# Kernel tuning notes

Hardware: AMD Instinct MI355X
Metric: run time of the kernel (lower is better)

Reference implementation:

```python
import jax, jax.numpy as jnp
import numpy as np

B, N, K = 64, 1024, 10   # graphs, nodes per graph, kNN neighbors
SLOPE = 0.01             # LeakyReLU default negative slope


def lrelu(v):
    return jnp.where(v >= 0, v, SLOPE * v)


def setup_inputs() -> dict:
    key = jax.random.key(0)
    ks = jax.random.split(key, 12)

    def w(k, shape):
        fan_in = shape[0]
        return jax.random.normal(k, shape, jnp.float32) * (1.0 / np.sqrt(fan_in))

    return {
        "x":   jax.random.normal(ks[0], (B * N, 1), jnp.float32),
        "pos": jax.random.normal(ks[1], (B * N, 3), jnp.float32),
        "tq":  jax.random.normal(ks[2], (B * N, 1), jnp.float32),
        # uniform, sorted graph assignment (B graphs of N nodes each)
        "batch": jnp.repeat(jnp.arange(B, dtype=jnp.int32), N),
        "W1":   w(ks[3], (10, 64)),  "b1":  jnp.zeros((64,), jnp.float32),
        "W2":   w(ks[4], (128, 64)), "b2":  jnp.zeros((64,), jnp.float32),
        "Wl1a": w(ks[5], (384, 512)), "bl1a": jnp.zeros((512,), jnp.float32),
        "Wl1b": w(ks[6], (512, 512)), "bl1b": jnp.zeros((512,), jnp.float32),
        "Wm1":  w(ks[7], (512, 256)), "bm1": jnp.zeros((256,), jnp.float32),
        "Wm2":  w(ks[8], (256, 3)),   "bm2": jnp.zeros((3,), jnp.float32),
    }


def _dynamic_edge_conv(h, W, b):
    # h: [B, N, F]. Dynamic kNN in feature space (per graph, self included,
    # matching PyG knn(x, x, k)), then sum_j LeakyReLU(Linear([x_i, x_j - x_i])).
    sq = jnp.sum(h * h, axis=-1)                                   # [B,N]
    dist = sq[:, :, None] + sq[:, None, :] - 2.0 * jnp.einsum("bif,bjf->bij", h, h)
    idx = jax.lax.top_k(-dist, K)[1]                               # [B,N,K] int32
    hj = jax.vmap(lambda hb, ib: hb[ib])(h, idx)                   # [B,N,K,F]
    hi = jnp.broadcast_to(h[:, :, None, :], hj.shape)
    e = jnp.concatenate([hi, hj - hi], axis=-1)                    # [B,N,K,2F]
    msg = lrelu(jnp.einsum("bnkf,fo->bnko", e, W) + b)             # [B,N,K,64]
    return jnp.sum(msg, axis=2)                                    # 'add' aggregation


def reference(x, pos, tq, batch, W1, b1, W2, b2,
              Wl1a, bl1a, Wl1b, bl1b, Wm1, bm1, Wm2, bm2):
    # batch is uniform & sorted: reshape to [B, N, .] realizes per-graph grouping.
    xx = jnp.concatenate([tq, x, pos], axis=1).reshape(B, N, 5)
    h1 = _dynamic_edge_conv(xx, W1, b1)
    h2 = _dynamic_edge_conv(h1, W2, b2)   # conv2 reused with shared weights
    h3 = _dynamic_edge_conv(h2, W2, b2)
    h4 = _dynamic_edge_conv(h3, W2, b2)
    h5 = _dynamic_edge_conv(h4, W2, b2)
    h6 = _dynamic_edge_conv(h5, W2, b2)
    hc = jnp.concatenate([h1, h2, h3, h4, h5, h6], axis=-1)        # [B,N,384]
    out0 = lrelu(hc @ Wl1a + bl1a) @ Wl1b + bl1b                   # [B,N,512]
    pooled = jnp.max(out0, axis=1)                                 # global_max_pool -> [B,512]
    return lrelu(pooled @ Wm1 + bm1) @ Wm2 + bm2                   # [B,3]
```

## Files before the change

### kernel.cpp

```cpp
#include <hip/hip_runtime.h>
#include <cstdint>
#include <cstddef>

constexpr int Bg = 64;
constexpr int Nn = 1024;
constexpr int Kk = 10;
constexpr int BN = Bg * Nn;
#define SLOPE 0.01f

typedef __attribute__((ext_vector_type(8))) short s16x8;
typedef __attribute__((ext_vector_type(4))) float f32x4;

__device__ __forceinline__ float lrelu(float v) { return v >= 0.f ? v : SLOPE * v; }

__device__ __forceinline__ unsigned encf(float f) {
  unsigned u = __float_as_uint(f);
  return (u & 0x80000000u) ? ~u : (u | 0x80000000u);
}
__device__ __forceinline__ float decf(unsigned e) {
  unsigned u = (e & 0x80000000u) ? (e & 0x7fffffffu) : ~e;
  return __uint_as_float(u);
}
__device__ __forceinline__ unsigned short f2bf(float f) {
  unsigned u = __float_as_uint(f);
  return (unsigned short)((u + 0x7FFFu + ((u >> 16) & 1u)) >> 16);
}
__device__ __forceinline__ float bf2f(unsigned short h) {
  return __uint_as_float(((unsigned)h) << 16);
}

__device__ __forceinline__ f32x4 mfma16(s16x8 a, s16x8 b, f32x4 c) {
  return __builtin_amdgcn_mfma_f32_16x16x32_bf16(a, b, c, 0, 0, 0);
}

__global__ __launch_bounds__(256) void pooled_init(unsigned* __restrict__ p) {
  p[blockIdx.x * 256 + threadIdx.x] = 0u;
}

__global__ __launch_bounds__(256) void build_xx(const float* __restrict__ x,
                                                const float* __restrict__ pos,
                                                const float* __restrict__ tq,
                                                float* __restrict__ xx,
                                                float* __restrict__ sqn, int rowoff) {
  int n = blockIdx.x * 256 + threadIdx.x;
  int g = rowoff + n;
  float v0 = tq[g], v1 = x[g];
  float v2 = pos[g * 3 + 0], v3 = pos[g * 3 + 1], v4 = pos[g * 3 + 2];
  xx[n * 5 + 0] = v0;
  xx[n * 5 + 1] = v1;
  xx[n * 5 + 2] = v2;
  xx[n * 5 + 3] = v3;
  xx[n * 5 + 4] = v4;
  float s0 = v0 * v0, s1 = v1 * v1, s2 = v2 * v2, s3 = v3 * v3, s4 = v4 * v4;
  sqn[n] = ((s0 + s4) + s2) + (s1 + s3);
}

template <int K>
__global__ __launch_bounds__(256) void wprep(const float* __restrict__ W,
                                             short* __restrict__ WH,
                                             short* __restrict__ WL) {
  int idx = blockIdx.x * 256 + threadIdx.x;
  int k = idx >> 9, n = idx & 511;
  float v = W[idx];
  unsigned short h = f2bf(v);
  unsigned short lo = f2bf(v - bf2f(h));
  WH[(size_t)n * K + k] = (short)h;
  WL[(size_t)n * K + k] = (short)lo;
}

template <int F>
__global__ __launch_bounds__(256) void uv_kernel(const float* __restrict__ h,
                                                 const float* __restrict__ W,
                                                 float* __restrict__ U,
                                                 float* __restrict__ V) {
  __shared__ float Ws[2 * F * 64];
  __shared__ float hs[16 * F];
  const int t = threadIdx.x;
  const int n0 = blockIdx.x * 16;
  for (int l = t; l < 2 * F * 64; l += 256) Ws[l] = W[l];
  for (int l = t; l < 16 * F; l += 256) hs[l] = h[(size_t)n0 * F + l];
  __syncthreads();
  for (int l = t; l < F * 64; l += 256) Ws[l] = Ws[l] - Ws[F * 64 + l];
  __syncthreads();
  const int o = t & 63;
  #pragma unroll
  for (int g4 = 0; g4 < 16; g4 += 4) {
    const int g = g4 + (t >> 6);
    float u = 0.f, v = 0.f;
    for (int f = 0; f < F; ++f) {
      float hv = hs[g * F + f];
      u += hv * Ws[f * 64 + o];
      v += hv * Ws[F * 64 + f * 64 + o];
    }
    U[(size_t)(n0 + g) * 64 + o] = u;
    V[(size_t)(n0 + g) * 64 + o] = v;
  }
}

#define LADDER_STATE                                                                     \
  float bd0 = INFINITY, bd1 = INFINITY, bd2 = INFINITY, bd3 = INFINITY, bd4 = INFINITY,  \
        bd5 = INFINITY, bd6 = INFINITY, bd7 = INFINITY, bd8 = INFINITY, bd9 = INFINITY;  \
  int bj0 = 0x7fffffff, bj1 = 0x7fffffff, bj2 = 0x7fffffff, bj3 = 0x7fffffff,            \
      bj4 = 0x7fffffff, bj5 = 0x7fffffff, bj6 = 0x7fffffff, bj7 = 0x7fffffff,            \
      bj8 = 0x7fffffff, bj9 = 0x7fffffff;

#define LADDER_INS                                                                        \
  auto ins = [&](float kd, int kj) {                                                      \
    bool m0 = kd < bd0; bool m1 = kd < bd1; bool m2 = kd < bd2; bool m3 = kd < bd3;       \
    bool m4 = kd < bd4; bool m5 = kd < bd5; bool m6 = kd < bd6; bool m7 = kd < bd7;       \
    bool m8 = kd < bd8; bool m9 = kd < bd9;                                               \
    bd9 = m8 ? bd8 : (m9 ? kd : bd9); bj9 = m8 ? bj8 : (m9 ? kj : bj9);                   \
    bd8 = m7 ? bd7 : (m8 ? kd : bd8); bj8 = m7 ? bj7 : (m8 ? kj : bj8);                   \
    bd7 = m6 ? bd6 : (m7 ? kd : bd7); bj7 = m6 ? bj6 : (m7 ? kj : bj7);                   \
    bd6 = m5 ? bd5 : (m6 ? kd : bd6); bj6 = m5 ? bj5 : (m6 ? kj : bj6);                   \
    bd5 = m4 ? bd4 : (m5 ? kd : bd5); bj5 = m4 ? bj4 : (m5 ? kj : bj5);                   \
    bd4 = m3 ? bd3 : (m4 ? kd : bd4); bj4 = m3 ? bj3 : (m4 ? kj : bj4);                   \
    bd3 = m2 ? bd2 : (m3 ? kd : bd3); bj3 = m2 ? bj2 : (m3 ? kj : bj3);                   \
    bd2 = m1 ? bd1 : (m2 ? kd : bd2); bj2 = m1 ? bj1 : (m2 ? kj : bj2);                   \
    bd1 = m0 ? bd0 : (m1 ? kd : bd1); bj1 = m0 ? bj0 : (m1 ? kj : bj1);                   \
    bd0 = m0 ? kd : bd0;              bj0 = m0 ? kj : bj0;                                \
  };

#define FMA16(av, bv)                                                        \
  do {                                                                       \
    acc[0][0] += av.x * bv.x; acc[0][1] += av.x * bv.y;                      \
    acc[0][2] += av.x * bv.z; acc[0][3] += av.x * bv.w;                      \
    acc[1][0] += av.y * bv.x; acc[1][1] += av.y * bv.y;                      \
    acc[1][2] += av.y * bv.z; acc[1][3] += av.y * bv.w;                      \
    acc[2][0] += av.z * bv.x; acc[2][1] += av.z * bv.y;                      \
    acc[2][2] += av.z * bv.z; acc[2][3] += av.z * bv.w;                      \
    acc[3][0] += av.w * bv.x; acc[3][1] += av.w * bv.y;                      \
    acc[3][2] += av.w * bv.z; acc[3][3] += av.w * bv.w;                      \
  } while (0)

template <int F>
__global__ __launch_bounds__(256) void knn_kernel(const float* __restrict__ h,
                                                  const float* __restrict__ sqn,
                                                  int* __restrict__ idxout) {
  constexpr int IPB = 64;
  constexpr int TJ = 64;
  constexpr int LDA = 68;
  constexpr int LDD = 65;
  constexpr int LDM = 41;
  constexpr int UNI = (IPB * LDM * 2 > TJ * LDA) ? IPB * LDM * 2 : TJ * LDA;
  __shared__ float As[F][LDA];
  __shared__ float uni[UNI];
  __shared__ float sqt[TJ];
  float* Bs = uni;
  float* D  = uni;
  float* md = uni;
  int*   mi = (int*)(uni + IPB * LDM);

  const int b = blockIdx.y;
  const int i0 = blockIdx.x * IPB;
  const int t = threadIdx.x;
  const int tx = t & 15, ty = t >> 4;
  const int gbase = b * Nn;
  const int r = t & 63;
  const int s = t >> 6;

  for (int l = t; l < IPB * F; l += 256) {
    int row = l / F, f = l % F;
    As[f][row] = h[(size_t)(gbase + i0 + row) * F + f];
  }

  LADDER_STATE
  LADDER_INS

  for (int jt = 0; jt < Nn; jt += TJ) {
    __syncthreads();
    for (int l = t; l < TJ * F; l += 256) {
      int row = l / F, f = l % F;
      Bs[f * LDA + row] = h[(size_t)(gbase + jt + row) * F + f];
    }
    if (t < TJ) sqt[t] = sqn[gbase + jt + t];
    __syncthreads();

    float acc[4][4] = {{0.f, 0.f, 0.f, 0.f}, {0.f, 0.f, 0.f, 0.f},
                       {0.f, 0.f, 0.f, 0.f}, {0.f, 0.f, 0.f, 0.f}};
    #pragma unroll
    for (int f = 0; f < F; ++f) {
      float4 av = *(const float4*)&As[f][ty * 4];
      float4 bv = *(const float4*)(Bs + f * LDA + tx * 4);
      FMA16(av, bv);
    }
    __syncthreads();

    float4 sj = *(const float4*)&sqt[tx * 4];
    #pragma unroll
    for (int ii = 0; ii < 4; ++ii) {
      float* dr = D + (ty * 4 + ii) * LDD + tx * 4;
      dr[0] = sj.x - 2.f * acc[ii][0];
      dr[1] = sj.y - 2.f * acc[ii][1];
      dr[2] = sj.z - 2.f * acc[ii][2];
      dr[3] = sj.w - 2.f * acc[ii][3];
    }
    __syncthreads();

    {
      const float* drow = D + r * LDD + s * 16;
      float dv[16];
      #pragma unroll
      for (int qq = 0; qq < 16; ++qq) dv[qq] = drow[qq];
      #pragma unroll
      for (int qq = 0; qq < 16; ++qq) ins(dv[qq], jt + s * 16 + qq);
    }
  }

  __syncthreads();
  {
    float* rd = md + r * LDM + s * 10;
    int*   ri = mi + r * LDM + s * 10;
    rd[0] = bd0; rd[1] = bd1; rd[2] = bd2; rd[3] = bd3; rd[4] = bd4;
    rd[5] = bd5; rd[6] = bd6; rd[7] = bd7; rd[8] = bd8; rd[9] = bd9;
    ri[0] = bj0; ri[1] = bj1; ri[2] = bj2; ri[3] = bj3; ri[4] = bj4;
    ri[5] = bj5; ri[6] = bj6; ri[7] = bj7; ri[8] = bj8; ri[9] = bj9;
  }
  __syncthreads();
  if (s == 0) {
    float* rd = md + r * LDM;
    int*   ri = mi + r * LDM;
    #pragma unroll 1
    for (int q = 0; q < Kk; ++q) {
      float best = INFINITY;
      int besti = 0x7fffffff, bslot = 0;
      #pragma unroll 1
      for (int e = 0; e < 40; ++e) {
        float d = rd[e];
        int ix = ri[e];
        bool g = (d < best) || (d == best && ix < besti);
        if (g) { best = d; besti = ix; bslot = e; }
      }
      rd[bslot] = INFINITY;
      idxout[(size_t)(gbase + i0 + r) * Kk + q] = besti;
    }
  }
}

__global__ __launch_bounds__(256) void knn64_mfma(const short* __restrict__ hH,
                                                  const short* __restrict__ hL,
                                                  const float* __restrict__ sqn,
                                                  int* __restrict__ idxout) {
  constexpr int LDB = 72;
  constexpr int LDD = 65;
  constexpr int LDM = 41;
  __shared__ float uni[64 * LDM * 2];
  __shared__ float sqt[64];
  short* BHs = (short*)uni;
  short* BLs = (short*)uni + 64 * LDB;
  float* D   = uni;
  float* md  = uni;
  int*   mi  = (int*)(uni + 64 * LDM);

  const int b = blockIdx.y;
  const int i0 = blockIdx.x * 64;
  const int t = threadIdx.x;
  const int w = t >> 6, l = t & 63;
  const int rl = l & 15, kb = l >> 4;
  const int gbase = b * Nn;

  s16x8 aH0, aH1, aL0, aL1;
  {
    const size_t ar = (size_t)(gbase + i0 + w * 16 + rl) * 64;
    aH0 = *(const s16x8*)&hH[ar + kb * 8];
    aH1 = *(const s16x8*)&hH[ar + 32 + kb * 8];
    aL0 = *(const s16x8*)&hL[ar + kb * 8];
    aL1 = *(const s16x8*)&hL[ar + 32 + kb * 8];
  }

  LADDER_STATE
  LADDER_INS

  uint4 pH0, pH1, pL0, pL1;
  {
    const size_t rb = (size_t)(gbase + l) * 64;
    pH0 = *(const uint4*)&hH[rb + w * 8];
    pH1 = *(const uint4*)&hH[rb + (w + 4) * 8];
    pL0 = *(const uint4*)&hL[rb + w * 8];
    pL1 = *(const uint4*)&hL[rb + (w + 4) * 8];
  }

  for (int jt = 0; jt < Nn; jt += 64) {
    __syncthreads();
    *(uint4*)&BHs[l * LDB + w * 8]       = pH0;
    *(uint4*)&BHs[l * LDB + (w + 4) * 8] = pH1;
    *(uint4*)&BLs[l * LDB + w * 8]       = pL0;
    *(uint4*)&BLs[l * LDB + (w + 4) * 8] = pL1;
    if (t < 64) sqt[t] = sqn[gbase + jt + t];
    if (jt + 64 < Nn) {
      const size_t rb = (size_t)(gbase + jt + 64 + l) * 64;
      pH0 = *(const uint4*)&hH[rb + w * 8];
      pH1 = *(const uint4*)&hH[rb + (w + 4) * 8];
      pL0 = *(const uint4*)&hL[rb + w * 8];
      pL1 = *(const uint4*)&hL[rb + (w + 4) * 8];
    }
    __syncthreads();

    f32x4 acc[4];
    #pragma unroll
    for (int cg = 0; cg < 4; ++cg) acc[cg] = (f32x4){0.f, 0.f, 0.f, 0.f};
    #pragma unroll
    for (int cg = 0; cg < 4; ++cg) {
      const int co = (cg * 16 + rl) * LDB;
      s16x8 bh0 = *(const s16x8*)&BHs[co + kb * 8];
      s16x8 bh1 = *(const s16x8*)&BHs[co + 32 + kb * 8];
      s16x8 bl0 = *(const s16x8*)&BLs[co + kb * 8];
      s16x8 bl1 = *(const s16x8*)&BLs[co + 32 + kb * 8];
      acc[cg] = mfma16(aH0, bh0, acc[cg]);
      acc[cg] = mfma16(aH0, bl0, acc[cg]);
      acc[cg] = mfma16(aL0, bh0, acc[cg]);
      acc[cg] = mfma16(aL0, bl0, acc[cg]);
      acc[cg] = mfma16(aH1, bh1, acc[cg]);
      acc[cg] = mfma16(aH1, bl1, acc[cg]);
      acc[cg] = mfma16(aL1, bh1, acc[cg]);
      acc[cg] = mfma16(aL1, bl1, acc[cg]);
    }
    __syncthreads();

    #pragma unroll
    for (int cg = 0; cg < 4; ++cg) {
      float sj = sqt[cg * 16 + rl];
      float* dp = D + (w * 16 + kb * 4) * LDD + cg * 16 + rl;
      dp[0 * LDD] = sj - 2.f * acc[cg][0];
      dp[1 * LDD] = sj - 2.f * acc[cg][1];
      dp[2 * LDD] = sj - 2.f * acc[cg][2];
      dp[3 * LDD] = sj - 2.f * acc[cg][3];
    }
    __syncthreads();

    {
      const float* drow = D + l * LDD + w * 16;
      float dv[16];
      #pragma unroll
      for (int qq = 0; qq < 16; ++qq) dv[qq] = drow[qq];
      #pragma unroll
      for (int qq = 0; qq < 16; ++qq) ins(dv[qq], jt + w * 16 + qq);
    }
  }

  __syncthreads();
  {
    float* rd = md + l * LDM + w * 10;
    int*   ri = mi + l * LDM + w * 10;
    rd[0] = bd0; rd[1] = bd1; rd[2] = bd2; rd[3] = bd3; rd[4] = bd4;
    rd[5] = bd5; rd[6] = bd6; rd[7] = bd7; rd[8] = bd8; rd[9] = bd9;
    ri[0] = bj0; ri[1] = bj1; ri[2] = bj2; ri[3] = bj3; ri[4] = bj4;
    ri[5] = bj5; ri[6] = bj6; ri[7] = bj7; ri[8] = bj8; ri[9] = bj9;
  }
  __syncthreads();
  if (w == 0) {
    float* rd = md + l * LDM;
    int*   ri = mi + l * LDM;
    #pragma unroll 1
    for (int q = 0; q < Kk; ++q) {
      float best = INFINITY;
      int besti = 0x7fffffff, bslot = 0;
      #pragma unroll 1
      for (int e = 0; e < 40; ++e) {
        float d = rd[e];
        int ix = ri[e];
        bool g = (d < best) || (d == best && ix < besti);
        if (g) { best = d; besti = ix; bslot = e; }
      }
      rd[bslot] = INFINITY;
      idxout[(size_t)(gbase + i0 + l) * Kk + q] = besti;
    }
  }
}

template <bool FUSE>
__global__ __launch_bounds__(256) void aggF_kernel(const float* __restrict__ U,
                                                   const float* __restrict__ V,
                                                   const int* __restrict__ idx,
                                                   const float* __restrict__ bias,
                                                   short* __restrict__ hH,
                                                   short* __restrict__ hL,
                                                   const float* __restrict__ W,
                                                   float* __restrict__ Uo,
                                                   float* __restrict__ Vo,
                                                   float* __restrict__ sqno) {
  __shared__ float Ws[FUSE ? 2 * 64 * 64 : 1];
  __shared__ float hs[FUSE ? 64 : 1][68];
  __shared__ float prt[FUSE ? 64 : 1][4];
  const int t = threadIdx.x;
  const int n0 = blockIdx.x * 64;
  const int r = t >> 2, s = t & 3, o0 = s * 16;
  const int n = n0 + r;
  const int gb = n & ~(Nn - 1);

  if constexpr (FUSE) {
    for (int l = t; l < 2 * 64 * 64; l += 256) Ws[l] = W[l];
  }

  float4 u[4], bb[4], acc[4];
  #pragma unroll
  for (int q = 0; q < 4; ++q) {
    u[q] = *(const float4*)&U[(size_t)n * 64 + o0 + q * 4];
    bb[q] = *(const float4*)&bias[o0 + q * 4];
    acc[q] = make_float4(0.f, 0.f, 0.f, 0.f);
  }
  #pragma unroll
  for (int k = 0; k < Kk; ++k) {
    int j = gb + idx[n * Kk + k];
    #pragma unroll
    for (int q = 0; q < 4; ++q) {
      float4 v = *(const float4*)&V[(size_t)j * 64 + o0 + q * 4];
      acc[q].x += lrelu(u[q].x + v.x + bb[q].x);
      acc[q].y += lrelu(u[q].y + v.y + bb[q].y);
      acc[q].z += lrelu(u[q].z + v.z + bb[q].z);
      acc[q].w += lrelu(u[q].w + v.w + bb[q].w);
    }
  }
  #pragma unroll
  for (int q = 0; q < 4; ++q) {
    ushort4 hv, lv;
    hv.x = f2bf(acc[q].x); lv.x = f2bf(acc[q].x - bf2f(hv.x));
    hv.y = f2bf(acc[q].y); lv.y = f2bf(acc[q].y - bf2f(hv.y));
    hv.z = f2bf(acc[q].z); lv.z = f2bf(acc[q].z - bf2f(hv.z));
    hv.w = f2bf(acc[q].w); lv.w = f2bf(acc[q].w - bf2f(hv.w));
    *(ushort4*)&hH[(size_t)n * 64 + o0 + q * 4] = hv;
    *(ushort4*)&hL[(size_t)n * 64 + o0 + q * 4] = lv;
  }
  if constexpr (!FUSE) return;

  #pragma unroll
  for (int q = 0; q < 4; ++q) *(float4*)&hs[r][o0 + q * 4] = acc[q];
  {
    float p = 0.f;
    #pragma unroll
    for (int q = 0; q < 4; ++q) {
      p += acc[q].x * acc[q].x;
      p += acc[q].y * acc[q].y;
      p += acc[q].z * acc[q].z;
      p += acc[q].w * acc[q].w;
    }
    prt[r][s] = p;
  }
  __syncthreads();
  for (int l = t; l < 64 * 64; l += 256) Ws[l] = Ws[l] - Ws[64 * 64 + l];
  if (s == 0) sqno[n] = ((prt[r][0] + prt[r][1]) + prt[r][2]) + prt[r][3];
  __syncthreads();

  const int o = t & 63;
  for (int g4 = 0; g4 < 64; g4 += 4) {
    const int g = g4 + (t >> 6);
    float uu = 0.f, vv = 0.f;
    for (int f = 0; f < 64; ++f) {
      float hv = hs[g][f];
      uu += hv * Ws[f * 64 + o];
      vv += hv * Ws[64 * 64 + f * 64 + o];
    }
    Uo[(size_t)(n0 + g) * 64 + o] = uu;
    Vo[(size_t)(n0 + g) * 64 + o] = vv;
  }
}

template <int MODE>
__global__ __launch_bounds__(256) void mfma_gemm(const short* __restrict__ AH,
                                                 const short* __restrict__ AL,
                                                 const short* __restrict__ BH,
                                                 const short* __restrict__ BL,
                                                 const float* __restrict__ bias,
                                                 short* __restrict__ outH,
                                                 short* __restrict__ outL,
                                                 unsigned* __restrict__ pooled,
                                                 int Msl, int zc, int g0) {
  constexpr int Kdim = (MODE == 0) ? 384 : 512;
  __shared__ short AHs[128][40], ALs[128][40], BHs[128][40], BLs[128][40];
  __shared__ float red[8][132];
  const int t = threadIdx.x;
  const int m0 = blockIdx.y * 128, n0 = blockIdx.x * 128;
  const int w = t >> 6, l = t & 63;
  const int q = w >> 1, p = w & 1, rl = l & 15, kb = l >> 4;
  const int srow = t >> 1, sc = (t & 1) * 16;

  f32x4 acc[4][4];
  #pragma unroll
  for (int m = 0; m < 4; ++m)
    #pragma unroll
    for (int n = 0; n < 4; ++n) acc[m][n] = (f32x4){0.f, 0.f, 0.f, 0.f};

  for (int k0 = 0; k0 < Kdim; k0 += 32) {
    size_t aoff, boff;
    if constexpr (MODE == 0)
      aoff = ((size_t)(k0 >> 6) * Msl + zc + m0 + srow) * 64 + (k0 & 63) + sc;
    else
      aoff = (size_t)(m0 + srow) * 512 + k0 + sc;
    boff = (size_t)(n0 + srow) * Kdim + k0 + sc;
    __syncthreads();
    *(uint4*)&AHs[srow][sc]     = *(const uint4*)(AH + aoff);
    *(uint4*)&AHs[srow][sc + 8] = *(const uint4*)(AH + aoff + 8);
    *(uint4*)&ALs[srow][sc]     = *(const uint4*)(AL + aoff);
    *(uint4*)&ALs[srow][sc + 8] = *(const uint4*)(AL + aoff + 8);
    *(uint4*)&BHs[srow][sc]     = *(const uint4*)(BH + boff);
    *(uint4*)&BHs[srow][sc + 8] = *(const uint4*)(BH + boff + 8);
    *(uint4*)&BLs[srow][sc]     = *(const uint4*)(BL + boff);
    *(uint4*)&BLs[srow][sc + 8] = *(const uint4*)(BL + boff + 8);
    __syncthreads();

    s16x8 aH[4], aL[4], bH[4], bL[4];
    #pragma unroll
    for (int m = 0; m < 4; ++m) {
      aH[m] = *(const s16x8*)&AHs[q * 64 + m * 16 + rl][kb * 8];
      aL[m] = *(const s16x8*)&ALs[q * 64 + m * 16 + rl][kb * 8];
    }
    #pragma unroll
    for (int n = 0; n < 4; ++n) {
      bH[n] = *(const s16x8*)&BHs[p * 64 + n * 16 + rl][kb * 8];
      bL[n] = *(const s16x8*)&BLs[p * 64 + n * 16 + rl][kb * 8];
    }
    #pragma unroll
    for (int m = 0; m < 4; ++m)
      #pragma unroll
      for (int n = 0; n < 4; ++n) {
        acc[m][n] = mfma16(aH[m], bH[n], acc[m][n]);
        acc[m][n] = mfma16(aH[m], bL[n], acc[m][n]);
        acc[m][n] = mfma16(aL[m], bH[n], acc[m][n]);
      }
  }

  if constexpr (MODE == 0) {
    #pragma unroll
    for (int n = 0; n < 4; ++n) {
      const int col = n0 + p * 64 + n * 16 + rl;
      const float bv = bias[col];
      #pragma unroll
      for (int m = 0; m < 4; ++m) {
        #pragma unroll
        for (int rr = 0; rr < 4; ++rr) {
          int row = m0 + q * 64 + m * 16 + kb * 4 + rr;
          float v = lrelu(acc[m][n][rr] + bv);
          unsigned short hv = f2bf(v);
          unsigned short lv = f2bf(v - bf2f(hv));
          outH[(size_t)row * 512 + col] = (short)hv;
          outL[(size_t)row * 512 + col] = (short)lv;
        }
      }
    }
  } else {
    #pragma unroll
    for (int n = 0; n < 4; ++n) {
      float cm = acc[0][n][0];
      #pragma unroll
      for (int m = 0; m < 4; ++m)
        #pragma unroll
        for (int rr = 0; rr < 4; ++rr) cm = fmaxf(cm, acc[m][n][rr]);
      red[q * 4 + kb][p * 64 + n * 16 + rl] = cm;
    }
    __syncthreads();
    if (t < 128) {
      float m = red[0][t];
      #pragma unroll
      for (int rr = 1; rr < 8; ++rr) m = fmaxf(m, red[rr][t]);
      m += bias[n0 + t];
      int g = g0 + ((zc + m0) >> 10);
      atomicMax(&pooled[(size_t)g * 512 + n0 + t], encf(m));
    }
  }
}

__global__ __launch_bounds__(256) void head_kernel(const unsigned* __restrict__ pooled,
                                                   const float* __restrict__ Wm1,
                                                   const float* __restrict__ bm1,
                                                   const float* __restrict__ Wm2,
                                                   const float* __restrict__ bm2,
                                                   float* __restrict__ out) {
  __shared__ float ps[512];
  __shared__ float hs[256];
  int b = blockIdx.x;
  int t = threadIdx.x;
  for (int l = t; l < 512; l += 256) ps[l] = decf(pooled[(size_t)b * 512 + l]);
  __syncthreads();
  float acc = bm1[t];
  for (int f = 0; f < 512; ++f) acc += ps[f] * Wm1[f * 256 + t];
  hs[t] = lrelu(acc);
  __syncthreads();
  if (t < 3) {
    float y = bm2[t];
    for (int f = 0; f < 256; ++f) y += hs[f] * Wm2[f * 3 + t];
    out[b * 3 + t] = y;
  }
}

static inline size_t al256(size_t v) { return (v + 255) & ~(size_t)255; }

extern "C" void kernel_launch(void* const* d_in, const int* in_sizes, int n_in,
                              void* d_out, int out_size, void* d_ws, size_t ws_size,
                              hipStream_t stream) {
  (void)in_sizes; (void)n_in; (void)out_size;
  const float* x    = (const float*)d_in[0];
  const float* pos  = (const float*)d_in[1];
  const float* tq   = (const float*)d_in[2];
  const float* W1   = (const float*)d_in[4];
  const float* b1   = (const float*)d_in[5];
  const float* W2   = (const float*)d_in[6];
  const float* b2   = (const float*)d_in[7];
  const float* Wl1a = (const float*)d_in[8];
  const float* bl1a = (const float*)d_in[9];
  const float* Wl1b = (const float*)d_in[10];
  const float* bl1b = (const float*)d_in[11];
  const float* Wm1  = (const float*)d_in[12];
  const float* bm1  = (const float*)d_in[13];
  const float* Wm2  = (const float*)d_in[14];
  const float* bm2  = (const float*)d_in[15];
  float* out = (float*)d_out;

  auto calc = [&](int G, size_t& hHB, size_t& uvB, size_t& uvzB) -> size_t {
    size_t M = (size_t)G * Nn;
    hHB = al256(M * 384 * 2);
    uvB = al256(M * 64 * 4);
    size_t Mz = M < 16384 ? M : 16384;
    size_t zB = 2 * al256(Mz * 512 * 2);
    uvzB = (4 * uvB > zB) ? 4 * uvB : zB;
    size_t convS = al256(M * 5 * 4) + al256(M * 4) + al256(M * Kk * 4);
    size_t wB = 2 * al256((size_t)512 * 384 * 2) + 2 * al256((size_t)512 * 512 * 2);
    return 2 * hHB + uvzB + convS + al256((size_t)Bg * 512 * 4) + wB + 1024;
  };
  int G = 64;
  size_t hHB = 0, uvB = 0, uvzB = 0;
  while (G > 1 && calc(G, hHB, uvB, uvzB) > ws_size) G >>= 1;
  calc(G, hHB, uvB, uvzB);
  const int M = G * Nn;
  const int Mz = M < 16384 ? M : 16384;

  char* w = (char*)d_ws;
  short* hH = (short*)w;
  short* hL = (short*)(w + hHB);
  char*  uvz = w + 2 * hHB;
  float* Ua = (float*)uvz;
  float* Va = (float*)(uvz + uvB);
  float* Ub = (float*)(uvz + 2 * uvB);
  float* Vb = (float*)(uvz + 3 * uvB);
  short* zH = (short*)uvz;
  short* zL = (short*)(uvz + al256((size_t)Mz * 512 * 2));
  char*  conv = uvz + uvzB;
  float* xx  = (float*)conv;
  float* sqn = (float*)(conv + al256((size_t)M * 5 * 4));
  int*   idx = (int*)((char*)sqn + al256((size_t)M * 4));
  unsigned* pooled = (unsigned*)((char*)idx + al256((size_t)M * Kk * 4));
  short* WHa = (short*)((char*)pooled + al256((size_t)Bg * 512 * 4));
  short* WLa = WHa + (size_t)512 * 384;
  short* WHb = (short*)((char*)WHa + 2 * al256((size_t)512 * 384 * 2));
  short* WLb = WHb + (size_t)512 * 512;

  wprep<384><<<(384 * 512) / 256, 256, 0, stream>>>(Wl1a, WHa, WLa);
  wprep<512><<<(512 * 512) / 256, 256, 0, stream>>>(Wl1b, WHb, WLb);
  pooled_init<<<(Bg * 512) / 256, 256, 0, stream>>>(pooled);

  for (int g0 = 0; g0 < Bg; g0 += G) {
    build_xx<<<M / 256, 256, 0, stream>>>(x, pos, tq, xx, sqn, g0 * Nn);

    uv_kernel<5><<<M / 16, 256, 0, stream>>>(xx, W1, Ua, Va);
    knn_kernel<5><<<dim3(Nn / 64, G), 256, 0, stream>>>(xx, sqn, idx);

    float *Ui = Ua, *Vi = Va, *Uo = Ub, *Vo = Vb;
    aggF_kernel<true><<<M / 64, 256, 0, stream>>>(Ui, Vi, idx, b1, hH, hL,
                                                  W2, Uo, Vo, sqn);
    { float* tp = Ui; Ui = Uo; Uo = tp; tp = Vi; Vi = Vo; Vo = tp; }

    for (int c = 1; c < 6; ++c) {
      knn64_mfma<<<dim3(Nn / 64, G), 256, 0, stream>>>(hH + (size_t)(c - 1) * M * 64,
                                                       hL + (size_t)(c - 1) * M * 64,
                                                       sqn, idx);
      if (c < 5) {
        aggF_kernel<true><<<M / 64, 256, 0, stream>>>(Ui, Vi, idx, b2,
                                                      hH + (size_t)c * M * 64,
                                                      hL + (size_t)c * M * 64,
                                                      W2, Uo, Vo, sqn);
        { float* tp = Ui; Ui = Uo; Uo = tp; tp = Vi; Vi = Vo; Vo = tp; }
      } else {
        aggF_kernel<false><<<M / 64, 256, 0, stream>>>(Ui, Vi, idx, b2,
                                                       hH + (size_t)5 * M * 64,
                                                       hL + (size_t)5 * M * 64,
                                                       nullptr, nullptr, nullptr, nullptr);
      }
    }

    for (int zc = 0; zc < M; zc += Mz) {
      mfma_gemm<0><<<dim3(4, Mz / 128), 256, 0, stream>>>(hH, hL, WHa, WLa, bl1a,
                                                          zH, zL, nullptr, M, zc, 0);
      mfma_gemm<1><<<dim3(4, Mz / 128), 256, 0, stream>>>(zH, zL, WHb, WLb, bl1b,
                                                          nullptr, nullptr, pooled, Mz, zc, g0);
    }
  }

  head_kernel<<<Bg, 256, 0, stream>>>(pooled, Wm1, bm1, Wm2, bm2, out);
}
```

Measured before the change: 1.564 ms.

## Double-buffer kNN tiles and insert distances straight from MFMA registers

Result: no change. 1.542 ms (-1.4%).

```diff
diff --git a/kernel.cpp b/kernel.cpp
--- a/kernel.cpp
+++ b/kernel.cpp
@@ -242,15 +242,11 @@
                                                   const float* __restrict__ sqn,
                                                   int* __restrict__ idxout) {
   constexpr int LDB = 72;
-  constexpr int LDD = 65;
   constexpr int LDM = 41;
-  __shared__ float uni[64 * LDM * 2];
-  __shared__ float sqt[64];
-  short* BHs = (short*)uni;
-  short* BLs = (short*)uni + 64 * LDB;
-  float* D   = uni;
-  float* md  = uni;
-  int*   mi  = (int*)(uni + 64 * LDM);
+  __shared__ __align__(16) short Bbuf[2][2][64 * LDB];
+  __shared__ float sqt[2][64];
+  float* md = (float*)&Bbuf[0][0][0];
+  int*   mi = (int*)(md + 64 * LDM);
 
   const int b = blockIdx.y;
   const int i0 = blockIdx.x * 64;
@@ -279,78 +275,135 @@
     pL0 = *(const uint4*)&hL[rb + w * 8];
     pL1 = *(const uint4*)&hL[rb + (w + 4) * 8];
   }
-
+  *(uint4*)&Bbuf[0][0][l * LDB + w * 8]       = pH0;
+  *(uint4*)&Bbuf[0][0][l * LDB + (w + 4) * 8] = pH1;
+  *(uint4*)&Bbuf[0][1][l * LDB + w * 8]       = pL0;
+  *(uint4*)&Bbuf[0][1][l * LDB + (w + 4) * 8] = pL1;
+  if (t < 64) sqt[0][t] = sqn[gbase + t];
+  {
+    const size_t rb = (size_t)(gbase + 64 + l) * 64;
+    pH0 = *(const uint4*)&hH[rb + w * 8];
+    pH1 = *(const uint4*)&hH[rb + (w + 4) * 8];
+    pL0 = *(const uint4*)&hL[rb + w * 8];
+    pL1 = *(const uint4*)&hL[rb + (w + 4) * 8];
+  }
+  __syncthreads();
+
+  int cur = 0;
   for (int jt = 0; jt < Nn; jt += 64) {
+    if (jt + 64 < Nn) {
+      short* BH1 = &Bbuf[cur ^ 1][0][0];
+      short* BL1 = &Bbuf[cur ^ 1][1][0];
+      *(uint4*)&BH1[l * LDB + w * 8]       = pH0;
+      *(uint4*)&BH1[l * LDB + (w + 4) * 8] = pH1;
+      *(uint4*)&BL1[l * LDB + w * 8]       = pL0;
+      *(uint4*)&BL1[l * LDB + (w + 4) * 8] = pL1;
+      if (t < 64) sqt[cur ^ 1][t] = sqn[gbase + jt + 64 + t];
+      if (jt + 128 < Nn) {
+        const size_t rb = (size_t)(gbase + jt + 128 + l) * 64;
+        pH0 = *(const uint4*)&hH[rb + w * 8];
+        pH1 = *(const uint4*)&hH[rb + (w + 4) * 8];
+        pL0 = *(const uint4*)&hL[rb + w * 8];
+        pL1 = *(const uint4*)&hL[rb + (w + 4) * 8];
+      }
+    }
+
+    const short* BH = &Bbuf[cur][0][0];
+    const short* BL = &Bbuf[cur][1][0];
+    f32x4 d0, d1, d2, d3;
+    {
+      const int co = (0 * 16 + rl) * LDB;
+      s16x8 bh0 = *(const s16x8*)&BH[co + kb * 8];
+      s16x8 bh1 = *(const s16x8*)&BH[co + 32 + kb * 8];
+      s16x8 bl0 = *(const s16x8*)&BL[co + kb * 8];
+      s16x8 bl1 = *(const s16x8*)&BL[co + 32 + kb * 8];
+      f32x4 a = (f32x4){0.f, 0.f, 0.f, 0.f};
+      a = mfma16(bh0, aH0, a); a = mfma16(bl0, aH0, a);
+      a = mfma16(bh0, aL0, a); a = mfma16(bl0, aL0, a);
+      a = mfma16(bh1, aH1, a); a = mfma16(bl1, aH1, a);
+      a = mfma16(bh1, aL1, a); a = mfma16(bl1, aL1, a);
+      d0 = a;
+    }
+    {
+      const int co = (1 * 16 + rl) * LDB;
+      s16x8 bh0 = *(const s16x8*)&BH[co + kb * 8];
+      s16x8 bh1 = *(const s16x8*)&BH[co + 32 + kb * 8];
+      s16x8 bl0 = *(const s16x8*)&BL[co + kb * 8];
+      s16x8 bl1 = *(const s16x8*)&BL[co + 32 + kb * 8];
+      f32x4 a = (f32x4){0.f, 0.f, 0.f, 0.f};
+      a = mfma16(bh0, aH0, a); a = mfma16(bl0, aH0, a);
+      a = mfma16(bh0, aL0, a); a = mfma16(bl0, aL0, a);
+      a = mfma16(bh1, aH1, a); a = mfma16(bl1, aH1, a);
+      a = mfma16(bh1, aL1, a); a = mfma16(bl1, aL1, a);
+      d1 = a;
+    }
+    {
+      const int co = (2 * 16 + rl) * LDB;
+      s16x8 bh0 = *(const s16x8*)&BH[co + kb * 8];
+      s16x8 bh1 = *(const s16x8*)&BH[co + 32 + kb * 8];
+      s16x8 bl0 = *(const s16x8*)&BL[co + kb * 8];
+      s16x8 bl1 = *(const s16x8*)&BL[co + 32 + kb * 8];
+      f32x4 a = (f32x4){0.f, 0.f, 0.f, 0.f};
+      a = mfma16(bh0, aH0, a); a = mfma16(bl0, aH0, a);
+      a = mfma16(bh0, aL0, a); a = mfma16(bl0, aL0, a);
+      a = mfma16(bh1, aH1, a); a = mfma16(bl1, aH1, a);
+      a = mfma16(bh1, aL1, a); a = mfma16(bl1, aL1, a);
+      d2 = a;
+    }
+    {
+      const int co = (3 * 16 + rl) * LDB;
+      s16x8 bh0 = *(const s16x8*)&BH[co + kb * 8];
+      s16x8 bh1 = *(const s16x8*)&BH[co + 32 + kb * 8];
+      s16x8 bl0 = *(const s16x8*)&BL[co + kb * 8];
+      s16x8 bl1 = *(const s16x8*)&BL[co + 32 + kb * 8];
+      f32x4 a = (f32x4){0.f, 0.f, 0.f, 0.f};
+      a = mfma16(bh0, aH0, a); a = mfma16(bl0, aH0, a);
+      a = mfma16(bh0, aL0, a); a = mfma16(bl0, aL0, a);
+      a = mfma16(bh1, aH1, a); a = mfma16(bl1, aH1, a);
+      a = mfma16(bh1, aL1, a); a = mfma16(bl1, aL1, a);
+      d3 = a;
+    }
+    {
+      float4 sj = *(const float4*)&sqt[cur][0 * 16 + kb * 4];
+      int jb = jt + 0 * 16 + kb * 4;
+      ins(sj.x - 2.f * d0[0], jb + 0); ins(sj.y - 2.f * d0[1], jb + 1);
+      ins(sj.z - 2.f * d0[2], jb + 2); ins(sj.w - 2.f * d0[3], jb + 3);
+    }
+    {
+      float4 sj = *(const float4*)&sqt[cur][1 * 16 + kb * 4];
+      int jb = jt + 1 * 16 + kb * 4;
+      ins(sj.x - 2.f * d1[0], jb + 0); ins(sj.y - 2.f * d1[1], jb + 1);
+      ins(sj.z - 2.f * d1[2], jb + 2); ins(sj.w - 2.f * d1[3], jb + 3);
+    }
+    {
+      float4 sj = *(const float4*)&sqt[cur][2 * 16 + kb * 4];
+      int jb = jt + 2 * 16 + kb * 4;
+      ins(sj.x - 2.f * d2[0], jb + 0); ins(sj.y - 2.f * d2[1], jb + 1);
+      ins(sj.z - 2.f * d2[2], jb + 2); ins(sj.w - 2.f * d2[3], jb + 3);
+    }
+    {
+      float4 sj = *(const float4*)&sqt[cur][3 * 16 + kb * 4];
+      int jb = jt + 3 * 16 + kb * 4;
+      ins(sj.x - 2.f * d3[0], jb + 0); ins(sj.y - 2.f * d3[1], jb + 1);
+      ins(sj.z - 2.f * d3[2], jb + 2); ins(sj.w - 2.f * d3[3], jb + 3);
+    }
     __syncthreads();
-    *(uint4*)&BHs[l * LDB + w * 8]       = pH0;
-    *(uint4*)&BHs[l * LDB + (w + 4) * 8] = pH1;
-    *(uint4*)&BLs[l * LDB + w * 8]       = pL0;
-    *(uint4*)&BLs[l * LDB + (w + 4) * 8] = pL1;
-    if (t < 64) sqt[t] = sqn[gbase + jt + t];
-    if (jt + 64 < Nn) {
-      const size_t rb = (size_t)(gbase + jt + 64 + l) * 64;
-      pH0 = *(const uint4*)&hH[rb + w * 8];
-      pH1 = *(const uint4*)&hH[rb + (w + 4) * 8];
-      pL0 = *(const uint4*)&hL[rb + w * 8];
-      pL1 = *(const uint4*)&hL[rb + (w + 4) * 8];
-    }
-    __syncthreads();
-
-    f32x4 acc[4];
-    #pragma unroll
-    for (int cg = 0; cg < 4; ++cg) acc[cg] = (f32x4){0.f, 0.f, 0.f, 0.f};
-    #pragma unroll
-    for (int cg = 0; cg < 4; ++cg) {
-      const int co = (cg * 16 + rl) * LDB;
-      s16x8 bh0 = *(const s16x8*)&BHs[co + kb * 8];
-      s16x8 bh1 = *(const s16x8*)&BHs[co + 32 + kb * 8];
-      s16x8 bl0 = *(const s16x8*)&BLs[co + kb * 8];
-      s16x8 bl1 = *(const s16x8*)&BLs[co + 32 + kb * 8];
-      acc[cg] = mfma16(aH0, bh0, acc[cg]);
-      acc[cg] = mfma16(aH0, bl0, acc[cg]);
-      acc[cg] = mfma16(aL0, bh0, acc[cg]);
-      acc[cg] = mfma16(aL0, bl0, acc[cg]);
-      acc[cg] = mfma16(aH1, bh1, acc[cg]);
-      acc[cg] = mfma16(aH1, bl1, acc[cg]);
-      acc[cg] = mfma16(aL1, bh1, acc[cg]);
-      acc[cg] = mfma16(aL1, bl1, acc[cg]);
-    }
-    __syncthreads();
-
-    #pragma unroll
-    for (int cg = 0; cg < 4; ++cg) {
-      float sj = sqt[cg * 16 + rl];
-      float* dp = D + (w * 16 + kb * 4) * LDD + cg * 16 + rl;
-      dp[0 * LDD] = sj - 2.f * acc[cg][0];
-      dp[1 * LDD] = sj - 2.f * acc[cg][1];
-      dp[2 * LDD] = sj - 2.f * acc[cg][2];
-      dp[3 * LDD] = sj - 2.f * acc[cg][3];
-    }
-    __syncthreads();
-
-    {
-      const float* drow = D + l * LDD + w * 16;
-      float dv[16];
-      #pragma unroll
-      for (int qq = 0; qq < 16; ++qq) dv[qq] = drow[qq];
-      #pragma unroll
-      for (int qq = 0; qq < 16; ++qq) ins(dv[qq], jt + w * 16 + qq);
-    }
-  }
-
-  __syncthreads();
+    cur ^= 1;
+  }
+
   {
-    float* rd = md + l * LDM + w * 10;
-    int*   ri = mi + l * LDM + w * 10;
+    const int row = w * 16 + rl;
+    float* rd = md + row * LDM + kb * 10;
+    int*   ri = mi + row * LDM + kb * 10;
     rd[0] = bd0; rd[1] = bd1; rd[2] = bd2; rd[3] = bd3; rd[4] = bd4;
     rd[5] = bd5; rd[6] = bd6; rd[7] = bd7; rd[8] = bd8; rd[9] = bd9;
     ri[0] = bj0; ri[1] = bj1; ri[2] = bj2; ri[3] = bj3; ri[4] = bj4;
     ri[5] = bj5; ri[6] = bj6; ri[7] = bj7; ri[8] = bj8; ri[9] = bj9;
   }
   __syncthreads();
-  if (w == 0) {
-    float* rd = md + l * LDM;
-    int*   ri = mi + l * LDM;
+  if (t < 64) {
+    float* rd = md + t * LDM;
+    int*   ri = mi + t * LDM;
     #pragma unroll 1
     for (int q = 0; q < Kk; ++q) {
       float best = INFINITY;
@@ -363,7 +416,7 @@
         if (g) { best = d; besti = ix; bslot = e; }
       }
       rd[bslot] = INFINITY;
-      idxout[(size_t)(gbase + i0 + l) * Kk + q] = besti;
+      idxout[(size_t)(gbase + i0 + t) * Kk + q] = besti;
     }
   }
 }
```

## Fuse kNN selection with edge aggregation and double-buffer candidate tiles

Applied to the files above, without the earlier changes.

After: 2.008 ms. 1.28x slower.

```diff
diff --git a/kernel.cpp b/kernel.cpp
--- a/kernel.cpp
+++ b/kernel.cpp
@@ -237,133 +237,224 @@
   }
 }
 
-__global__ __launch_bounds__(256) void knn64_mfma(const short* __restrict__ hH,
-                                                  const short* __restrict__ hL,
-                                                  const float* __restrict__ sqn,
-                                                  int* __restrict__ idxout) {
+template <bool FUSE>
+__global__ __launch_bounds__(256) void knnagg(const short* __restrict__ hHin,
+                                              const short* __restrict__ hLin,
+                                              const float* __restrict__ sqn,
+                                              const float* __restrict__ U,
+                                              const float* __restrict__ V,
+                                              const float* __restrict__ bias,
+                                              short* __restrict__ hHout,
+                                              short* __restrict__ hLout,
+                                              const float* __restrict__ W,
+                                              float* __restrict__ Uo,
+                                              float* __restrict__ Vo,
+                                              float* __restrict__ sqno) {
   constexpr int LDB = 72;
-  constexpr int LDD = 65;
   constexpr int LDM = 41;
-  __shared__ float uni[64 * LDM * 2];
-  __shared__ float sqt[64];
-  short* BHs = (short*)uni;
-  short* BLs = (short*)uni + 64 * LDB;
-  float* D   = uni;
-  float* md  = uni;
-  int*   mi  = (int*)(uni + 64 * LDM);
+  __shared__ __align__(16) char pool[2 * 2 * 64 * LDB * 2];
+  __shared__ float sqt[2][64];
+  __shared__ float hs[FUSE ? 64 : 1][68];
+  __shared__ float prt[FUSE ? 64 : 1][4];
+  __shared__ int idx_s[64][10];
+  float* md = (float*)pool;
+  int*   mi = (int*)(md + 64 * LDM);
+  float* Ws = (float*)pool;
 
   const int b = blockIdx.y;
   const int i0 = blockIdx.x * 64;
   const int t = threadIdx.x;
-  const int w = t >> 6, l = t & 63;
-  const int rl = l & 15, kb = l >> 4;
   const int gbase = b * Nn;
 
-  s16x8 aH0, aH1, aL0, aL1;
   {
-    const size_t ar = (size_t)(gbase + i0 + w * 16 + rl) * 64;
-    aH0 = *(const s16x8*)&hH[ar + kb * 8];
-    aH1 = *(const s16x8*)&hH[ar + 32 + kb * 8];
-    aL0 = *(const s16x8*)&hL[ar + kb * 8];
-    aL1 = *(const s16x8*)&hL[ar + 32 + kb * 8];
-  }
-
-  LADDER_STATE
-  LADDER_INS
-
-  uint4 pH0, pH1, pL0, pL1;
+    const int w = t >> 6, l = t & 63;
+    const int rl = l & 15, kb = l >> 4;
+    auto Bp = [&](int buf, int plane) -> short* {
+      return (short*)pool + ((size_t)buf * 2 + plane) * 64 * LDB;
+    };
+
+    s16x8 aH0, aH1, aL0, aL1;
+    {
+      const size_t ar = (size_t)(gbase + i0 + w * 16 + rl) * 64;
+      aH0 = *(const s16x8*)&hHin[ar + kb * 8];
+      aH1 = *(const s16x8*)&hHin[ar + 32 + kb * 8];
+      aL0 = *(const s16x8*)&hLin[ar + kb * 8];
+      aL1 = *(const s16x8*)&hLin[ar + 32 + kb * 8];
+    }
+
+    LADDER_STATE
+    LADDER_INS
+
+    uint4 pH0, pH1, pL0, pL1;
+    {
+      const size_t rb = (size_t)(gbase + l) * 64;
+      pH0 = *(const uint4*)&hHin[rb + w * 8];
+      pH1 = *(const uint4*)&hHin[rb + (w + 4) * 8];
+      pL0 = *(const uint4*)&hLin[rb + w * 8];
+      pL1 = *(const uint4*)&hLin[rb + (w + 4) * 8];
+    }
+    *(uint4*)&Bp(0, 0)[l * LDB + w * 8]       = pH0;
+    *(uint4*)&Bp(0, 0)[l * LDB + (w + 4) * 8] = pH1;
+    *(uint4*)&Bp(0, 1)[l * LDB + w * 8]       = pL0;
+    *(uint4*)&Bp(0, 1)[l * LDB + (w + 4) * 8] = pL1;
+    if (t < 64) sqt[0][t] = sqn[gbase + t];
+    {
+      const size_t rb = (size_t)(gbase + 64 + l) * 64;
+      pH0 = *(const uint4*)&hHin[rb + w * 8];
+      pH1 = *(const uint4*)&hHin[rb + (w + 4) * 8];
+      pL0 = *(const uint4*)&hLin[rb + w * 8];
+      pL1 = *(const uint4*)&hLin[rb + (w + 4) * 8];
+    }
+    __syncthreads();
+
+    int cur = 0;
+    for (int jt = 0; jt < Nn; jt += 64) {
+      if (jt + 64 < Nn) {
+        short* BH1 = Bp(cur ^ 1, 0);
+        short* BL1 = Bp(cur ^ 1, 1);
+        *(uint4*)&BH1[l * LDB + w * 8]       = pH0;
+        *(uint4*)&BH1[l * LDB + (w + 4) * 8] = pH1;
+        *(uint4*)&BL1[l * LDB + w * 8]       = pL0;
+        *(uint4*)&BL1[l * LDB + (w + 4) * 8] = pL1;
+        if (t < 64) sqt[cur ^ 1][t] = sqn[gbase + jt + 64 + t];
+        if (jt + 128 < Nn) {
+          const size_t rb = (size_t)(gbase + jt + 128 + l) * 64;
+          pH0 = *(const uint4*)&hHin[rb + w * 8];
+          pH1 = *(const uint4*)&hHin[rb + (w + 4) * 8];
+          pL0 = *(const uint4*)&hLin[rb + w * 8];
+          pL1 = *(const uint4*)&hLin[rb + (w + 4) * 8];
+        }
+      }
+
+      const short* BH = Bp(cur, 0);
+      const short* BL = Bp(cur, 1);
+      f32x4 dists[4];
+      #pragma unroll
+      for (int cg = 0; cg < 4; ++cg) {
+        const int co = (cg * 16 + rl) * LDB;
+        s16x8 bh0 = *(const s16x8*)&BH[co + kb * 8];
+        s16x8 bh1 = *(const s16x8*)&BH[co + 32 + kb * 8];
+        s16x8 bl0 = *(const s16x8*)&BL[co + kb * 8];
+        s16x8 bl1 = *(const s16x8*)&BL[co + 32 + kb * 8];
+        f32x4 a = (f32x4){0.f, 0.f, 0.f, 0.f};
+        a = mfma16(bh0, aH0, a); a = mfma16(bl0, aH0, a);
+        a = mfma16(bh0, aL0, a); a = mfma16(bl0, aL0, a);
+        a = mfma16(bh1, aH1, a); a = mfma16(bl1, aH1, a);
+        a = mfma16(bh1, aL1, a); a = mfma16(bl1, aL1, a);
+        dists[cg] = a;
+      }
+      #pragma unroll
+      for (int cg = 0; cg < 4; ++cg) {
+        float4 sj = *(const float4*)&sqt[cur][cg * 16 + kb * 4];
+        int jb = jt + cg * 16 + kb * 4;
+        ins(sj.x - 2.f * dists[cg][0], jb + 0);
+        ins(sj.y - 2.f * dists[cg][1], jb + 1);
+        ins(sj.z - 2.f * dists[cg][2], jb + 2);
+        ins(sj.w - 2.f * dists[cg][3], jb + 3);
+      }
+      __syncthreads();
+      cur ^= 1;
+    }
+
+    {
+      const int row = w * 16 + rl;
+      float* rd = md + row * LDM + kb * 10;
+      int*   ri = mi + row * LDM + kb * 10;
+      rd[0] = bd0; rd[1] = bd1; rd[2] = bd2; rd[3] = bd3; rd[4] = bd4;
+      rd[5] = bd5; rd[6] = bd6; rd[7] = bd7; rd[8] = bd8; rd[9] = bd9;
+      ri[0] = bj0; ri[1] = bj1; ri[2] = bj2; ri[3] = bj3; ri[4] = bj4;
+      ri[5] = bj5; ri[6] = bj6; ri[7] = bj7; ri[8] = bj8; ri[9] = bj9;
+    }
+    __syncthreads();
+    if (t < 64) {
+      float* rd = md + t * LDM;
+      int*   ri = mi + t * LDM;
+      #pragma unroll 1
+      for (int q = 0; q < Kk; ++q) {
+        float best = INFINITY;
+        int besti = 0x7fffffff, bslot = 0;
+        #pragma unroll 1
+        for (int e = 0; e < 40; ++e) {
+          float d = rd[e];
+          int ix = ri[e];
+          bool g = (d < best) || (d == best && ix < besti);
+          if (g) { best = d; besti = ix; bslot = e; }
+        }
+        rd[bslot] = INFINITY;
+        idx_s[t][q] = besti;
+      }
+    }
+    __syncthreads();
+  }
+
   {
-    const size_t rb = (size_t)(gbase + l) * 64;
-    pH0 = *(const uint4*)&hH[rb + w * 8];
-    pH1 = *(const uint4*)&hH[rb + (w + 4) * 8];
-    pL0 = *(const uint4*)&hL[rb + w * 8];
-    pL1 = *(const uint4*)&hL[rb + (w + 4) * 8];
-  }
-
-  for (int jt = 0; jt < Nn; jt += 64) {
-    __syncthreads();
-    *(uint4*)&BHs[l * LDB + w * 8]       = pH0;
-    *(uint4*)&BHs[l * LDB + (w + 4) * 8] = pH1;
-    *(uint4*)&BLs[l * LDB + w * 8]       = pL0;
-    *(uint4*)&BLs[l * LDB + (w + 4) * 8] = pL1;
-    if (t < 64) sqt[t] = sqn[gbase + jt + t];
-    if (jt + 64 < Nn) {
-      const size_t rb = (size_t)(gbase + jt + 64 + l) * 64;
-      pH0 = *(const uint4*)&hH[rb + w * 8];
-      pH1 = *(const uint4*)&hH[rb + (w + 4) * 8];
-      pL0 = *(const uint4*)&hL[rb + w * 8];
-      pL1 = *(const uint4*)&hL[rb + (w + 4) * 8];
-    }
-    __syncthreads();
-
-    f32x4 acc[4];
-    #pragma unroll
-    for (int cg = 0; cg < 4; ++cg) acc[cg] = (f32x4){0.f, 0.f, 0.f, 0.f};
-    #pragma unroll
-    for (int cg = 0; cg < 4; ++cg) {
-      const int co = (cg * 16 + rl) * LDB;
-      s16x8 bh0 = *(const s16x8*)&BHs[co + kb * 8];
-      s16x8 bh1 = *(const s16x8*)&BHs[co + 32 + kb * 8];
-      s16x8 bl0 = *(const s16x8*)&BLs[co + kb * 8];
-      s16x8 bl1 = *(const s16x8*)&BLs[co + 32 + kb * 8];
-      acc[cg] = mfma16(aH0, bh0, acc[cg]);
-      acc[cg] = mfma16(aH0, bl0, acc[cg]);
-      acc[cg] = mfma16(aL0, bh0, acc[cg]);
-      acc[cg] = mfma16(aL0, bl0, acc[cg]);
-      acc[cg] = mfma16(aH1, bh1, acc[cg]);
-      acc[cg] = mfma16(aH1, bl1, acc[cg]);
-      acc[cg] = mfma16(aL1, bh1, acc[cg]);
-      acc[cg] = mfma16(aL1, bl1, acc[cg]);
-    }
-    __syncthreads();
-
-    #pragma unroll
-    for (int cg = 0; cg < 4; ++cg) {
-      float sj = sqt[cg * 16 + rl];
-      float* dp = D + (w * 16 + kb * 4) * LDD + cg * 16 + rl;
-      dp[0 * LDD] = sj - 2.f * acc[cg][0];
-      dp[1 * LDD] = sj - 2.f * acc[cg][1];
-      dp[2 * LDD] = sj - 2.f * acc[cg][2];
-      dp[3 * LDD] = sj - 2.f * acc[cg][3];
-    }
-    __syncthreads();
-
+    const int r = t >> 2, s = t & 3, o0 = s * 16;
+    const int n = gbase + i0 + r;
+
+    if constexpr (FUSE) {
+      for (int l = t; l < 2 * 64 * 64; l += 256) Ws[l] = W[l];
+    }
+
+    float4 u[4], bb[4], acc[4];
+    #pragma unroll
+    for (int q = 0; q < 4; ++q) {
+      u[q] = *(const float4*)&U[(size_t)n * 64 + o0 + q * 4];
+      bb[q] = *(const float4*)&bias[o0 + q * 4];
+      acc[q] = make_float4(0.f, 0.f, 0.f, 0.f);
+    }
+    #pragma unroll
+    for (int k = 0; k < Kk; ++k) {
+      int j = gbase + idx_s[r][k];
+      #pragma unroll
+      for (int q = 0; q < 4; ++q) {
+        float4 v = *(const float4*)&V[(size_t)j * 64 + o0 + q * 4];
+        acc[q].x += lrelu(u[q].x + v.x + bb[q].x);
+        acc[q].y += lrelu(u[q].y + v.y + bb[q].y);
+        acc[q].z += lrelu(u[q].z + v.z + bb[q].z);
+        acc[q].w += lrelu(u[q].w + v.w + bb[q].w);
+      }
+    }
+    #pragma unroll
+    for (int q = 0; q < 4; ++q) {
+      ushort4 hv, lv;
+      hv.x = f2bf(acc[q].x); lv.x = f2bf(acc[q].x - bf2f(hv.x));
+      hv.y = f2bf(acc[q].y); lv.y = f2bf(acc[q].y - bf2f(hv.y));
+      hv.z = f2bf(acc[q].z); lv.z = f2bf(acc[q].z - bf2f(hv.z));
+      hv.w = f2bf(acc[q].w); lv.w = f2bf(acc[q].w - bf2f(hv.w));
+      *(ushort4*)&hHout[(size_t)n * 64 + o0 + q * 4] = hv;
+      *(ushort4*)&hLout[(size_t)n * 64 + o0 + q * 4] = lv;
+    }
+    if constexpr (!FUSE) return;
+
+    #pragma unroll
+    for (int q = 0; q < 4; ++q) *(float4*)&hs[r][o0 + q * 4] = acc[q];
     {
-      const float* drow = D + l * LDD + w * 16;
-      float dv[16];
-      #pragma unroll
-      for (int qq = 0; qq < 16; ++qq) dv[qq] = drow[qq];
-      #pragma unroll
-      for (int qq = 0; qq < 16; ++qq) ins(dv[qq], jt + w * 16 + qq);
-    }
-  }
-
-  __syncthreads();
-  {
-    float* rd = md + l * LDM + w * 10;
-    int*   ri = mi + l * LDM + w * 10;
-    rd[0] = bd0; rd[1] = bd1; rd[2] = bd2; rd[3] = bd3; rd[4] = bd4;
-    rd[5] = bd5; rd[6] = bd6; rd[7] = bd7; rd[8] = bd8; rd[9] = bd9;
-    ri[0] = bj0; ri[1] = bj1; ri[2] = bj2; ri[3] = bj3; ri[4] = bj4;
-    ri[5] = bj5; ri[6] = bj6; ri[7] = bj7; ri[8] = bj8; ri[9] = bj9;
-  }
-  __syncthreads();
-  if (w == 0) {
-    float* rd = md + l * LDM;
-    int*   ri = mi + l * LDM;
-    #pragma unroll 1
-    for (int q = 0; q < Kk; ++q) {
-      float best = INFINITY;
-      int besti = 0x7fffffff, bslot = 0;
-      #pragma unroll 1
-      for (int e = 0; e < 40; ++e) {
-        float d = rd[e];
-        int ix = ri[e];
-        bool g = (d < best) || (d == best && ix < besti);
-        if (g) { best = d; besti = ix; bslot = e; }
-      }
-      rd[bslot] = INFINITY;
-      idxout[(size_t)(gbase + i0 + l) * Kk + q] = besti;
+      float p = 0.f;
+      #pragma unroll
+      for (int q = 0; q < 4; ++q) {
+        p += acc[q].x * acc[q].x;
+        p += acc[q].y * acc[q].y;
+        p += acc[q].z * acc[q].z;
+        p += acc[q].w * acc[q].w;
+      }
+      prt[r][s] = p;
+    }
+    __syncthreads();
+    for (int l = t; l < 64 * 64; l += 256) Ws[l] = Ws[l] - Ws[64 * 64 + l];
+    if (s == 0) sqno[n] = ((prt[r][0] + prt[r][1]) + prt[r][2]) + prt[r][3];
+    __syncthreads();
+
+    const int o = t & 63;
+    for (int g4 = 0; g4 < 64; g4 += 4) {
+      const int g = g4 + (t >> 6);
+      float uu = 0.f, vv = 0.f;
+      for (int f = 0; f < 64; ++f) {
+        float hv = hs[g][f];
+        uu += hv * Ws[f * 64 + o];
+        vv += hv * Ws[64 * 64 + f * 64 + o];
+      }
+      Uo[(size_t)(gbase + i0 + g) * 64 + o] = uu;
+      Vo[(size_t)(gbase + i0 + g) * 64 + o] = vv;
     }
   }
 }
@@ -487,15 +578,23 @@
     else
       aoff = (size_t)(m0 + srow) * 512 + k0 + sc;
     boff = (size_t)(n0 + srow) * Kdim + k0 + sc;
-    __syncthreads();
-    *(uint4*)&AHs[srow][sc]     = *(const uint4*)(AH + aoff);
-    *(uint4*)&AHs[srow][sc + 8] = *(const uint4*)(AH + aoff + 8);
-    *(uint4*)&ALs[srow][sc]     = *(const uint4*)(AL + aoff);
-    *(uint4*)&ALs[srow][sc + 8] = *(const uint4*)(AL + aoff + 8);
-    *(uint4*)&BHs[srow][sc]     = *(const uint4*)(BH + boff);
-    *(uint4*)&BHs[srow][sc + 8] = *(const uint4*)(BH + boff + 8);
-    *(uint4*)&BLs[srow][sc]     = *(const uint4*)(BL + boff);
-    *(uint4*)&BLs[srow][sc + 8] = *(const uint4*)(BL + boff + 8);
+    uint4 ga0 = *(const uint4*)(AH + aoff);
+    uint4 ga1 = *(const uint4*)(AH + aoff + 8);
+    uint4 gl0 = *(const uint4*)(AL + aoff);
+    uint4 gl1 = *(const uint4*)(AL + aoff + 8);
+    uint4 gb0 = *(const uint4*)(BH + boff);
+    uint4 gb1 = *(const uint4*)(BH + boff + 8);
+    uint4 gc0 = *(const uint4*)(BL + boff);
+    uint4 gc1 = *(const uint4*)(BL + boff + 8);
+    __syncthreads();
+    *(uint4*)&AHs[srow][sc]     = ga0;
+    *(uint4*)&AHs[srow][sc + 8] = ga1;
+    *(uint4*)&ALs[srow][sc]     = gl0;
+    *(uint4*)&ALs[srow][sc + 8] = gl1;
+    *(uint4*)&BHs[srow][sc]     = gb0;
+    *(uint4*)&BHs[srow][sc + 8] = gb1;
+    *(uint4*)&BLs[srow][sc]     = gc0;
+    *(uint4*)&BLs[srow][sc + 8] = gc1;
     __syncthreads();
 
     s16x8 aH[4], aL[4], bH[4], bL[4];
@@ -612,7 +711,7 @@
     size_t Mz = M < 16384 ? M : 16384;
     size_t zB = 2 * al256(Mz * 512 * 2);
     uvzB = (4 * uvB > zB) ? 4 * uvB : zB;
-    size_t convS = al256(M * 5 * 4) + al256(M * 4) + al256(M * Kk * 4);
+    size_t convS = al256(M * 5 * 4) + 2 * al256(M * 4) + al256(M * Kk * 4);
     size_t wB = 2 * al256((size_t)512 * 384 * 2) + 2 * al256((size_t)512 * 512 * 2);
     return 2 * hHB + uvzB + convS + al256((size_t)Bg * 512 * 4) + wB + 1024;
   };
@@ -634,9 +733,10 @@
   short* zH = (short*)uvz;
   short* zL = (short*)(uvz + al256((size_t)Mz * 512 * 2));
   char*  conv = uvz + uvzB;
-  float* xx  = (float*)conv;
-  float* sqn = (float*)(conv + al256((size_t)M * 5 * 4));
-  int*   idx = (int*)((char*)sqn + al256((size_t)M * 4));
+  float* xx   = (float*)conv;
+  float* sqnA = (float*)(conv + al256((size_t)M * 5 * 4));
+  float* sqnB = (float*)((char*)sqnA + al256((size_t)M * 4));
+  int*   idx  = (int*)((char*)sqnB + al256((size_t)M * 4));
   unsigned* pooled = (unsigned*)((char*)idx + al256((size_t)M * Kk * 4));
   short* WHa = (short*)((char*)pooled + al256((size_t)Bg * 512 * 4));
   short* WLa = WHa + (size_t)512 * 384;
@@ -648,31 +748,30 @@
   pooled_init<<<(Bg * 512) / 256, 256, 0, stream>>>(pooled);
 
   for (int g0 = 0; g0 < Bg; g0 += G) {
-    build_xx<<<M / 256, 256, 0, stream>>>(x, pos, tq, xx, sqn, g0 * Nn);
+    build_xx<<<M / 256, 256, 0, stream>>>(x, pos, tq, xx, sqnA, g0 * Nn);
 
     uv_kernel<5><<<M / 16, 256, 0, stream>>>(xx, W1, Ua, Va);
-    knn_kernel<5><<<dim3(Nn / 64, G), 256, 0, stream>>>(xx, sqn, idx);
-
-    float *Ui = Ua, *Vi = Va, *Uo = Ub, *Vo = Vb;
-    aggF_kernel<true><<<M / 64, 256, 0, stream>>>(Ui, Vi, idx, b1, hH, hL,
-                                                  W2, Uo, Vo, sqn);
-    { float* tp = Ui; Ui = Uo; Uo = tp; tp = Vi; Vi = Vo; Vo = tp; }
-
+    knn_kernel<5><<<dim3(Nn / 64, G), 256, 0, stream>>>(xx, sqnA, idx);
+    aggF_kernel<true><<<M / 64, 256, 0, stream>>>(Ua, Va, idx, b1, hH, hL,
+                                                  W2, Ub, Vb, sqnB);
+
+    float *Ui = Ub, *Vi = Vb, *Uo = Ua, *Vo = Va;
+    float *sqI = sqnB, *sqO = sqnA;
     for (int c = 1; c < 6; ++c) {
-      knn64_mfma<<<dim3(Nn / 64, G), 256, 0, stream>>>(hH + (size_t)(c - 1) * M * 64,
-                                                       hL + (size_t)(c - 1) * M * 64,
-                                                       sqn, idx);
+      const short* hHin = hH + (size_t)(c - 1) * M * 64;
+      const short* hLin = hL + (size_t)(c - 1) * M * 64;
+      short* hHout = hH + (size_t)c * M * 64;
+      short* hLout = hL + (size_t)c * M * 64;
       if (c < 5) {
-        aggF_kernel<true><<<M / 64, 256, 0, stream>>>(Ui, Vi, idx, b2,
-                                                      hH + (size_t)c * M * 64,
-                                                      hL + (size_t)c * M * 64,
-                                                      W2, Uo, Vo, sqn);
-        { float* tp = Ui; Ui = Uo; Uo = tp; tp = Vi; Vi = Vo; Vo = tp; }
+        knnagg<true><<<dim3(Nn / 64, G), 256, 0, stream>>>(hHin, hLin, sqI,
+                                                           Ui, Vi, b2, hHout, hLout,
+                                                           W2, Uo, Vo, sqO);
+        { float* tp = Ui; Ui = Uo; Uo = tp; tp = Vi; Vi = Vo; Vo = tp;
+          tp = sqI; sqI = sqO; sqO = tp; }
       } else {
-        aggF_kernel<false><<<M / 64, 256, 0, stream>>>(Ui, Vi, idx, b2,
-                                                       hH + (size_t)5 * M * 64,
-                                                       hL + (size_t)5 * M * 64,
-                                                       nullptr, nullptr, nullptr, nullptr);
+        knnagg<false><<<dim3(Nn / 64, G), 256, 0, stream>>>(hHin, hLin, sqI,
+                                                            Ui, Vi, b2, hHout, hLout,
+                                                            nullptr, nullptr, nullptr, nullptr);
       }
     }
 
```
